# Kernel tuning notes

Hardware: AMD Instinct MI355X
Metric: run time of the kernel (lower is better)

Reference implementation:

```python
import jax, jax.numpy as jnp
import numpy as np

B, C, T, F = 2, 256, 1024, 64
N, HID = 4, 64


def setup_inputs() -> dict:
    key = jax.random.key(0)
    ks = jax.random.split(key, 9)
    s = 0.02
    return {
        "x": jax.random.normal(ks[0], (B, C, T, F), dtype=jnp.float32),
        "Wq": jax.random.normal(ks[1], (N, HID, C), dtype=jnp.float32) * s,
        "bq": jnp.zeros((N, HID), dtype=jnp.float32),
        "Wk": jax.random.normal(ks[2], (N, HID, C), dtype=jnp.float32) * s,
        "bk": jnp.zeros((N, HID), dtype=jnp.float32),
        "Wv": jax.random.normal(ks[3], (N, C // N, C), dtype=jnp.float32) * s,
        "bv": jnp.zeros((N, C // N), dtype=jnp.float32),
        "Wp": jax.random.normal(ks[4], (C, C), dtype=jnp.float32) * s,
        "bp": jnp.zeros((C,), dtype=jnp.float32),
    }


def reference(x, Wq, bq, Wk, bk, Wv, bv, Wp, bp):
    b, c, t, f = x.shape
    n = Wq.shape[0]
    # conv1x1 per head then torch: cat(dim=0) -> [N*b, h, t, f]; transpose(1,2); flatten -> [N*b, t, h*f]
    def proj(W, bias):
        h = W.shape[1]
        y = jnp.einsum('bctf,nhc->nbthf', x, W) + bias[:, None, None, :, None]
        return y.reshape(n * b, t, h * f)

    Q = proj(Wq, bq)                       # [N*b, t, hid*f]
    K = proj(Wk, bk)                       # [N*b, t, hid*f]
    V = proj(Wv, bv)                       # [N*b, t, (c/N)*f]

    scale = 1.0 / jnp.sqrt(jnp.asarray(Q.shape[-1], dtype=x.dtype))
    attn = jax.nn.softmax(jnp.einsum('mte,mse->mts', Q, K) * scale, axis=2)
    Vo = jnp.einsum('mts,msd->mtd', attn, V)             # [N*b, t, c*f/N]

    # torch: reshape(b*N, t, c*f//N).transpose(1,2).view(N,b,c//N,t,f).transpose(0,1).view(b,c,t,f)
    Vo = Vo.transpose(0, 2, 1)                            # [N*b, c*f/N, t]
    Vo = Vo.reshape(n, b, c // n, t, f)
    Vo = jnp.swapaxes(Vo, 0, 1).reshape(b, c, t, f)

    out = jnp.einsum('bctf,oc->botf', Vo, Wp) + bp[None, :, None, None]
    return out + x
```

## Files before the change

kernel.cpp:

```cpp
#include <hip/hip_runtime.h>

#define DI __device__ __forceinline__

static constexpr int B_ = 2;
static constexpr int C_ = 256;
static constexpr int T_ = 1024;
static constexpr int F_ = 64;
static constexpr int M_ = 8;
static constexpr int E_ = 4096;
static constexpr float SCALE_ = 1.0f / 64.0f;

typedef __attribute__((ext_vector_type(8))) short bf16x8;
typedef __attribute__((ext_vector_type(4))) float f32x4;

DI unsigned short bf16_rne(float f) {
    unsigned int u = __float_as_uint(f);
    return (unsigned short)((u + 0x7FFFu + ((u >> 16) & 1u)) >> 16);
}
DI float bf2f(unsigned short h) { return __uint_as_float(((unsigned int)h) << 16); }
DI ushort4 pack4(float a, float b, float c, float d) {
    return make_ushort4(bf16_rne(a), bf16_rne(b), bf16_rne(c), bf16_rne(d));
}
DI float4 up4(ushort4 u) {
    return make_float4(bf2f(u.x), bf2f(u.y), bf2f(u.z), bf2f(u.w));
}

DI void gload_lds16(const unsigned short* g, unsigned short* l) {
    __builtin_amdgcn_global_load_lds(
        (const __attribute__((address_space(1))) unsigned int*)g,
        (__attribute__((address_space(3))) unsigned int*)l, 16, 0, 0);
}

DI void mfma16(f32x4& acc, bf16x8 a, bf16x8 b) {
    asm("v_mfma_f32_16x16x32_bf16 %0, %1, %2, %0" : "+v"(acc) : "v"(a), "v"(b));
}

__global__ __launch_bounds__(256) void wconv_kernel(
    const float* __restrict__ Wq, const float* __restrict__ Wk,
    const float* __restrict__ Wv, const float* __restrict__ Wp,
    const float* __restrict__ bq, const float* __restrict__ bk,
    const float* __restrict__ bv,
    unsigned short* __restrict__ Wall, unsigned short* __restrict__ Wpb,
    float* __restrict__ bias_all)
{
    const int tid = (int)threadIdx.x;
    const int bid = (int)blockIdx.x;
    if (bid < 192) {
        const int idx = (bid * 256 + tid) * 4;
        const int proj = idx >> 16, rem = idx & 65535;
        const float* src = proj == 0 ? Wq : (proj == 1 ? Wk : Wv);
        float4 v = *(const float4*)(src + rem);
        *(ushort4*)(Wall + idx) = pack4(v.x, v.y, v.z, v.w);
        const int gid = bid * 256 + tid;
        if (gid < 768) {
            float bb = gid < 256 ? bq[gid] : (gid < 512 ? bk[gid - 256] : bv[gid - 512]);
            bias_all[gid] = bb;
        }
    } else {
        const int idx = ((bid - 192) * 256 + tid) * 4;
        float4 v = *(const float4*)(Wp + idx);
        *(ushort4*)(Wpb + idx) = pack4(v.x, v.y, v.z, v.w);
    }
}

__global__ __launch_bounds__(256) void qkv_two(
    const float* __restrict__ x, const unsigned short* __restrict__ Wall,
    const float* __restrict__ bias_all, unsigned short* __restrict__ outQ)
{
    const int wgid = (int)blockIdx.x;
    const int b = wgid >> 10, tft = wgid & 1023;
    const int tfbase = tft * 64;

    const int tid = (int)threadIdx.x;
    const int wid = tid >> 6, lane = tid & 63;
    const int wr = wid >> 1, wc = wid & 1;
    const int lo16 = lane & 15, hi4 = lane >> 4;

    __shared__ unsigned short As[4 * 64 * 64];
    __shared__ unsigned short Bs[128 * 64];

    {
        const int a = lane & 3, cg = lane >> 2;
        const int rowb = wid * 16 + a * 4;
        const float* xb = x + (size_t)b * (C_ * T_ * F_) + tfbase + rowb;
        const size_t cstep = 65536;

        float4 va[4], vb[4];
#pragma unroll
        for (int g = 0; g < 4; ++g)
            va[g] = *(const float4*)(xb + (size_t)(cg * 4 + g) * cstep);

#pragma unroll
        for (int cb = 0; cb < 4; ++cb) {
            if (cb < 3) {
                const int c0n = (cb + 1) * 64 + cg * 4;
#pragma unroll
                for (int g = 0; g < 4; ++g)
                    vb[g] = *(const float4*)(xb + (size_t)(c0n + g) * cstep);
            }
#pragma unroll
            for (int j = 0; j < 4; ++j) {
                const int row = rowb + j;
                const int phys = row * 64 + (((cg >> 1) ^ (row & 7)) << 3) + (cg & 1) * 4;
                float e0 = (&va[0].x)[j], e1 = (&va[1].x)[j];
                float e2 = (&va[2].x)[j], e3 = (&va[3].x)[j];
                *(ushort4*)&As[cb * 4096 + phys] = pack4(e0, e1, e2, e3);
            }
#pragma unroll
            for (int g = 0; g < 4; ++g) va[g] = vb[g];
        }
    }

    const int srow = lane >> 3;
    const int scol = ((lane & 7) ^ srow) * 8;
    const int tf0 = tfbase + wr * 32;

    __syncthreads();

    for (int ntl = 0; ntl < 6; ++ntl) {
        const int nbase = ntl * 128;
        const unsigned short* brow = Wall + (size_t)nbase * 256;
        f32x4 acc[2][4] = {};

        for (int kc = 0; kc < 4; ++kc) {
#pragma unroll
            for (int i = 0; i < 4; ++i) {
                const int rb = wid * 32 + i * 8;
                gload_lds16(brow + (size_t)(rb + srow) * 256 + kc * 64 + scol,
                            &Bs[rb * 64]);
            }
            __syncthreads();
#pragma unroll
            for (int kk = 0; kk < 2; ++kk) {
                const int hc = (kk * 32 + hi4 * 8) ^ ((lane & 7) << 3);
                bf16x8 a[2], bb[4];
#pragma unroll
                for (int mi = 0; mi < 2; ++mi)
                    a[mi] = *(const bf16x8*)&As[kc * 4096 + (wr * 32 + mi * 16 + lo16) * 64 + hc];
#pragma unroll
                for (int nj = 0; nj < 4; ++nj)
                    bb[nj] = *(const bf16x8*)&Bs[(wc * 64 + nj * 16 + lo16) * 64 + hc];
#pragma unroll
                for (int mi = 0; mi < 2; ++mi)
#pragma unroll
                    for (int nj = 0; nj < 4; ++nj)
                        mfma16(acc[mi][nj], a[mi], bb[nj]);
            }
            __syncthreads();
        }

        asm volatile("s_nop 7\n\ts_nop 7" ::: "memory");
#pragma unroll
        for (int nj = 0; nj < 4; ++nj) {
            const int r_col = nbase + wc * 64 + nj * 16 + lo16;
            const int projl = r_col >> 8;
            const int rr = r_col & 255;
            const int mrow = (rr >> 6) * 2 + b;
            const int h = rr & 63;
            const float bv = bias_all[r_col];
            unsigned short* dst0 = outQ + (size_t)projl * 33554432
                                 + (size_t)mrow * (T_ * E_) + h * 64;
#pragma unroll
            for (int mi = 0; mi < 2; ++mi) {
                const int tf = tf0 + mi * 16 + hi4 * 4;
                const int t = tf >> 6, f = tf & 63;
                *(ushort4*)(dst0 + (size_t)t * E_ + f) =
                    pack4(acc[mi][nj][0] + bv, acc[mi][nj][1] + bv,
                          acc[mi][nj][2] + bv, acc[mi][nj][3] + bv);
            }
        }
    }
}

__global__ __launch_bounds__(256) void scores_mfma(
    const unsigned short* __restrict__ Q, const unsigned short* __restrict__ K,
    unsigned short* __restrict__ S)
{
    const int orig = (int)blockIdx.x;
    const int wg = (orig & 7) * 64 + (orig >> 3);
    const int m = wg >> 6;
    const int rest = wg & 63;
    const int sbase = (rest & 7) * 128;
    const int tbase = (rest >> 3) * 128;
    const int tid = (int)threadIdx.x;
    const int wid = tid >> 6, lane = tid & 63;
    const int wr = wid >> 1, wc = wid & 1;
    const int lo16 = lane & 15, hi4 = lane >> 4;

    __shared__ unsigned short As[128 * 64];
    __shared__ unsigned short Bs[128 * 64];

    f32x4 acc[4][4] = {};

    const unsigned short* qrow = Q + ((size_t)m * T_ + tbase) * E_;
    const unsigned short* krow = K + ((size_t)m * T_ + sbase) * E_;

    const int srow = lane >> 3;
    const int scol = ((lane & 7) ^ srow) * 8;

    for (int eb = 0; eb < E_; eb += 64) {
#pragma unroll
        for (int i = 0; i < 4; ++i) {
            const int rb = wid * 32 + i * 8;
            gload_lds16(qrow + (size_t)(rb + srow) * E_ + eb + scol, &As[rb * 64]);
            gload_lds16(krow + (size_t)(rb + srow) * E_ + eb + scol, &Bs[rb * 64]);
        }
        __syncthreads();
#pragma unroll
        for (int kk = 0; kk < 2; ++kk) {
            const int hc = (kk * 32 + hi4 * 8) ^ ((lane & 7) << 3);
            bf16x8 a[4], bb[4];
#pragma unroll
            for (int mi = 0; mi < 4; ++mi)
                a[mi] = *(const bf16x8*)&As[(wr * 64 + mi * 16 + lo16) * 64 + hc];
#pragma unroll
            for (int nj = 0; nj < 4; ++nj)
                bb[nj] = *(const bf16x8*)&Bs[(wc * 64 + nj * 16 + lo16) * 64 + hc];
#pragma unroll
            for (int mi = 0; mi < 4; ++mi)
#pragma unroll
                for (int nj = 0; nj < 4; ++nj)
                    mfma16(acc[mi][nj], a[mi], bb[nj]);
        }
        __syncthreads();
    }

    asm volatile("s_nop 7\n\ts_nop 7" ::: "memory");
#pragma unroll
    for (int mi = 0; mi < 4; ++mi)
#pragma unroll
        for (int r = 0; r < 4; ++r) {
            int trow = tbase + wr * 64 + mi * 16 + hi4 * 4 + r;
            unsigned short* sp = S + ((size_t)m * T_ + trow) * T_ + sbase + wc * 64 + lo16;
#pragma unroll
            for (int nj = 0; nj < 4; ++nj)
                sp[nj * 16] = bf16_rne(acc[mi][nj][r] * SCALE_);
        }
}

__global__ __launch_bounds__(256) void softmax_kernel(
    const unsigned short* __restrict__ S, unsigned short* __restrict__ A)
{
    const size_t rowoff = ((size_t)blockIdx.y * T_ + blockIdx.x) * T_;
    const int tid = (int)threadIdx.x;
    const int wid = tid >> 6, lane = tid & 63;

    __shared__ float redmx[4];
    __shared__ float redsm[4];

    float4 v = up4(*(const ushort4*)(S + rowoff + tid * 4));
    float mx = fmaxf(fmaxf(v.x, v.y), fmaxf(v.z, v.w));
#pragma unroll
    for (int off = 32; off > 0; off >>= 1) mx = fmaxf(mx, __shfl_xor(mx, off));
    if (lane == 0) redmx[wid] = mx;
    __syncthreads();
    mx = fmaxf(fmaxf(redmx[0], redmx[1]), fmaxf(redmx[2], redmx[3]));

    float e0 = __expf(v.x - mx), e1 = __expf(v.y - mx);
    float e2 = __expf(v.z - mx), e3 = __expf(v.w - mx);
    float sm = (e0 + e1) + (e2 + e3);
#pragma unroll
    for (int off = 32; off > 0; off >>= 1) sm += __shfl_xor(sm, off);
    if (lane == 0) redsm[wid] = sm;
    __syncthreads();
    sm = (redsm[0] + redsm[1]) + (redsm[2] + redsm[3]);
    float inv = 1.0f / sm;
    *(ushort4*)(A + rowoff + tid * 4) = pack4(e0 * inv, e1 * inv, e2 * inv, e3 * inv);
}

__global__ __launch_bounds__(256) void vt_kernel(
    const unsigned short* __restrict__ V, unsigned short* __restrict__ Vt)
{
    const int m = blockIdx.z;
    const int d0 = blockIdx.x * 64;
    const int s0 = blockIdx.y * 64;
    const int tid = (int)threadIdx.x;
    __shared__ unsigned short ts[64][68];

    const unsigned short* vp = V + (size_t)m * T_ * E_;
#pragma unroll
    for (int it = 0; it < 4; ++it) {
        int idx = it * 256 + tid;
        int sl = idx >> 4, d4 = (idx & 15) * 4;
        *(ushort4*)&ts[sl][d4] = *(const ushort4*)&vp[(size_t)(s0 + sl) * E_ + d0 + d4];
    }
    __syncthreads();
    unsigned short* op = Vt + (size_t)m * E_ * T_;
    const int dl = tid >> 2, s16 = (tid & 3) * 16;
#pragma unroll
    for (int q = 0; q < 4; ++q) {
        int s4 = s16 + q * 4;
        ushort4 v = make_ushort4(ts[s4][dl], ts[s4+1][dl], ts[s4+2][dl], ts[s4+3][dl]);
        *(ushort4*)&op[(size_t)(d0 + dl) * T_ + s0 + s4] = v;
    }
}

__global__ __launch_bounds__(256) void pv_mfma(
    const unsigned short* __restrict__ A, const unsigned short* __restrict__ Vt,
    unsigned short* __restrict__ G)
{
    const int orig = (int)blockIdx.x;
    const int wg = (orig & 7) * 256 + (orig >> 3);
    const int m = wg >> 8;
    const int rest = wg & 255;
    const int dbase = (rest & 31) * 128;
    const int tbase = (rest >> 5) * 128;
    const int nh = m >> 1, b = m & 1;
    const int tid = (int)threadIdx.x;
    const int wid = tid >> 6, lane = tid & 63;
    const int wr = wid >> 1, wc = wid & 1;
    const int lo16 = lane & 15, hi4 = lane >> 4;

    __shared__ unsigned short As[128 * 64];
    __shared__ unsigned short Bs[128 * 64];

    f32x4 acc[4][4] = {};

    const unsigned short* arow = A  + ((size_t)m * T_ + tbase) * T_;
    const unsigned short* vrow = Vt + (size_t)m * E_ * T_ + (size_t)dbase * T_;

    const int srow = lane >> 3;
    const int scol = ((lane & 7) ^ srow) * 8;

    for (int sb = 0; sb < T_; sb += 64) {
#pragma unroll
        for (int i = 0; i < 4; ++i) {
            const int rb = wid * 32 + i * 8;
            gload_lds16(arow + (size_t)(rb + srow) * T_ + sb + scol, &As[rb * 64]);
            gload_lds16(vrow + (size_t)(rb + srow) * T_ + sb + scol, &Bs[rb * 64]);
        }
        __syncthreads();
#pragma unroll
        for (int kk = 0; kk < 2; ++kk) {
            const int hc = (kk * 32 + hi4 * 8) ^ ((lane & 7) << 3);
            bf16x8 a[4], bb[4];
#pragma unroll
            for (int mi = 0; mi < 4; ++mi)
                a[mi] = *(const bf16x8*)&As[(wr * 64 + mi * 16 + lo16) * 64 + hc];
#pragma unroll
            for (int nj = 0; nj < 4; ++nj)
                bb[nj] = *(const bf16x8*)&Bs[(wc * 64 + nj * 16 + lo16) * 64 + hc];
#pragma unroll
            for (int mi = 0; mi < 4; ++mi)
#pragma unroll
                for (int nj = 0; nj < 4; ++nj)
                    mfma16(acc[mi][nj], a[mi], bb[nj]);
        }
        __syncthreads();
    }

    asm volatile("s_nop 7\n\ts_nop 7" ::: "memory");
    const int cb   = nh * 64 + (dbase >> 6) + wc;
    const int t2lo = (tbase >> 6) + wr;
#pragma unroll
    for (int mi = 0; mi < 4; ++mi) {
        const int tl = mi * 16 + hi4 * 4;
#pragma unroll
        for (int nj = 0; nj < 4; ++nj) {
            const int d63 = nj * 16 + lo16;
            size_t addr = (((size_t)(b * 256 + cb)) * 1024 + d63 * 16 + t2lo) * 64 + tl;
            *(ushort4*)&G[addr] = pack4(acc[mi][nj][0], acc[mi][nj][1],
                                        acc[mi][nj][2], acc[mi][nj][3]);
        }
    }
}

__global__ __launch_bounds__(256) void gt_kernel(
    const unsigned short* __restrict__ G, unsigned short* __restrict__ GT)
{
    const int tf0 = blockIdx.x * 64;
    const int c0  = blockIdx.y * 64;
    const int b   = blockIdx.z;
    const int tid = (int)threadIdx.x;
    __shared__ unsigned short ts[64][68];

    const unsigned short* gb = G + (size_t)(b * 256 + c0) * 65536 + tf0;
#pragma unroll
    for (int it = 0; it < 4; ++it) {
        int idx = it * 256 + tid;
        int cl = idx >> 4, tf4 = (idx & 15) * 4;
        *(ushort4*)&ts[cl][tf4] = *(const ushort4*)(gb + (size_t)cl * 65536 + tf4);
    }
    __syncthreads();
    const int tfl = tid >> 2, c16 = (tid & 3) * 16;
    unsigned short* op = GT + ((size_t)b * 65536 + tf0 + tfl) * 256 + c0 + c16;
#pragma unroll
    for (int q = 0; q < 4; ++q) {
        int cl = c16 + q * 4;
        ushort4 v = make_ushort4(ts[cl][tfl], ts[cl+1][tfl], ts[cl+2][tfl], ts[cl+3][tfl]);
        *(ushort4*)(op + q * 4) = v;
    }
}

__global__ __launch_bounds__(256) void outproj_mfma(
    const unsigned short* __restrict__ GT, const unsigned short* __restrict__ Wpb,
    const float* __restrict__ bp, const float* __restrict__ x,
    float* __restrict__ out)
{
    const int tfbase = blockIdx.x * 128;
    const int obase  = blockIdx.y * 128;
    const int b      = blockIdx.z;
    const int tid = (int)threadIdx.x;
    const int wid = tid >> 6, lane = tid & 63;
    const int wr = wid >> 1, wc = wid & 1;
    const int lo16 = lane & 15, hi4 = lane >> 4;

    __shared__ unsigned short As[128 * 64];
    __shared__ unsigned short Bs[128 * 64];

    f32x4 acc[4][4] = {};

    const unsigned short* arow = GT + ((size_t)b * 65536 + tfbase) * 256;
    const unsigned short* brow = Wpb + (size_t)obase * 256;

    const int srow = lane >> 3;
    const int scol = ((lane & 7) ^ srow) * 8;

    for (int cb = 0; cb < 256; cb += 64) {
#pragma unroll
        for (int i = 0; i < 4; ++i) {
            const int rb = wid * 32 + i * 8;
            gload_lds16(arow + (size_t)(rb + srow) * 256 + cb + scol, &As[rb * 64]);
            gload_lds16(brow + (size_t)(rb + srow) * 256 + cb + scol, &Bs[rb * 64]);
        }
        __syncthreads();
#pragma unroll
        for (int kk = 0; kk < 2; ++kk) {
            const int hc = (kk * 32 + hi4 * 8) ^ ((lane & 7) << 3);
            bf16x8 a[4], bb[4];
#pragma unroll
            for (int mi = 0; mi < 4; ++mi)
                a[mi] = *(const bf16x8*)&As[(wr * 64 + mi * 16 + lo16) * 64 + hc];
#pragma unroll
            for (int nj = 0; nj < 4; ++nj)
                bb[nj] = *(const bf16x8*)&Bs[(wc * 64 + nj * 16 + lo16) * 64 + hc];
#pragma unroll
            for (int mi = 0; mi < 4; ++mi)
#pragma unroll
                for (int nj = 0; nj < 4; ++nj)
                    mfma16(acc[mi][nj], a[mi], bb[nj]);
        }
        __syncthreads();
    }

    asm volatile("s_nop 7\n\ts_nop 7" ::: "memory");
#pragma unroll
    for (int nj = 0; nj < 4; ++nj) {
        const int o = obase + wc * 64 + nj * 16 + lo16;
        const float bias = bp[o];
        const size_t rowb = ((size_t)(b * 256 + o)) * 65536;
#pragma unroll
        for (int mi = 0; mi < 4; ++mi) {
            const int tf = tfbase + wr * 64 + mi * 16 + hi4 * 4;
            float4 xv = *(const float4*)(x + rowb + tf);
            float4 r = make_float4(acc[mi][nj][0] + bias + xv.x,
                                   acc[mi][nj][1] + bias + xv.y,
                                   acc[mi][nj][2] + bias + xv.z,
                                   acc[mi][nj][3] + bias + xv.w);
            *(float4*)(out + rowb + tf) = r;
        }
    }
}

extern "C" void kernel_launch(void* const* d_in, const int* in_sizes, int n_in,
                              void* d_out, int out_size, void* d_ws, size_t ws_size,
                              hipStream_t stream) {
    const float* x  = (const float*)d_in[0];
    const float* Wq = (const float*)d_in[1];
    const float* bq = (const float*)d_in[2];
    const float* Wk = (const float*)d_in[3];
    const float* bk = (const float*)d_in[4];
    const float* Wv = (const float*)d_in[5];
    const float* bv = (const float*)d_in[6];
    const float* Wp = (const float*)d_in[7];
    const float* bp = (const float*)d_in[8];
    float* out = (float*)d_out;

    char* ws = (char*)d_ws;
    unsigned short* Q    = (unsigned short*)(ws);
    unsigned short* K    = (unsigned short*)(ws + 67108864);
    unsigned short* V    = (unsigned short*)(ws + 134217728);
    unsigned short* S    = (unsigned short*)(ws + 201326592);
    unsigned short* A    = (unsigned short*)(ws + 218103808);
    unsigned short* Wall = (unsigned short*)(ws + 234881024);
    float* bias_all      = (float*)(ws + 235274240);
    unsigned short* Wpb  = (unsigned short*)(ws + 235277312);
    unsigned short* Vt = K;
    unsigned short* G  = Q;
    unsigned short* GT = V;

    wconv_kernel<<<256, 256, 0, stream>>>(Wq, Wk, Wv, Wp, bq, bk, bv, Wall, Wpb, bias_all);
    qkv_two<<<2048, 256, 0, stream>>>(x, Wall, bias_all, Q);
    scores_mfma<<<512, 256, 0, stream>>>(Q, K, S);
    softmax_kernel<<<dim3(T_, M_), 256, 0, stream>>>(S, A);
    vt_kernel<<<dim3(64, 16, M_), 256, 0, stream>>>(V, Vt);
    pv_mfma<<<2048, 256, 0, stream>>>(A, Vt, G);
    gt_kernel<<<dim3(1024, 4, 2), 256, 0, stream>>>(G, GT);
    outproj_mfma<<<dim3(512, 2, 2), 256, 0, stream>>>(GT, Wpb, bp, x, out);
}
```

Baseline: 417.4 us.

## Load QKV weight fragments directly from global into registers, drop LDS B tile

The QKV projection kernel no longer stages weight tiles in shared memory. Each wave now owns 32 output columns across all 64 rows, reading its bf16 weight fragments straight from global/L2 into registers. This removes the LDS staging loads and both barriers per k-chunk. In exchange it loses cross-wave sharing of the B tile, relying on cache for the weight reads, and uses a different accumulator shape (4x2 instead of 2x4).

```diff
diff --git a/kernel.cpp b/kernel.cpp
--- a/kernel.cpp
+++ b/kernel.cpp
@@ -63,7 +63,7 @@
     }
 }
 
-__global__ __launch_bounds__(256) void qkv_two(
+__global__ __launch_bounds__(256) void qkv_three(
     const float* __restrict__ x, const unsigned short* __restrict__ Wall,
     const float* __restrict__ bias_all, unsigned short* __restrict__ outQ)
 {
@@ -73,11 +73,9 @@
 
     const int tid = (int)threadIdx.x;
     const int wid = tid >> 6, lane = tid & 63;
-    const int wr = wid >> 1, wc = wid & 1;
     const int lo16 = lane & 15, hi4 = lane >> 4;
 
     __shared__ unsigned short As[4 * 64 * 64];
-    __shared__ unsigned short Bs[128 * 64];
 
     {
         const int a = lane & 3, cg = lane >> 2;
@@ -111,48 +109,41 @@
         }
     }
 
-    const int srow = lane >> 3;
-    const int scol = ((lane & 7) ^ srow) * 8;
-    const int tf0 = tfbase + wr * 32;
-
     __syncthreads();
 
     for (int ntl = 0; ntl < 6; ++ntl) {
         const int nbase = ntl * 128;
-        const unsigned short* brow = Wall + (size_t)nbase * 256;
-        f32x4 acc[2][4] = {};
+        const unsigned short* wbase =
+            Wall + ((size_t)(nbase + wid * 32 + lo16)) * 256 + hi4 * 8;
+        f32x4 acc[4][2] = {};
 
         for (int kc = 0; kc < 4; ++kc) {
-#pragma unroll
-            for (int i = 0; i < 4; ++i) {
-                const int rb = wid * 32 + i * 8;
-                gload_lds16(brow + (size_t)(rb + srow) * 256 + kc * 64 + scol,
-                            &Bs[rb * 64]);
-            }
-            __syncthreads();
+            bf16x8 bfr[2][2];
+#pragma unroll
+            for (int kk = 0; kk < 2; ++kk)
+#pragma unroll
+                for (int nj = 0; nj < 2; ++nj)
+                    bfr[kk][nj] = *(const bf16x8*)(wbase + (size_t)nj * 16 * 256
+                                                   + kc * 64 + kk * 32);
 #pragma unroll
             for (int kk = 0; kk < 2; ++kk) {
                 const int hc = (kk * 32 + hi4 * 8) ^ ((lane & 7) << 3);
-                bf16x8 a[2], bb[4];
-#pragma unroll
-                for (int mi = 0; mi < 2; ++mi)
-                    a[mi] = *(const bf16x8*)&As[kc * 4096 + (wr * 32 + mi * 16 + lo16) * 64 + hc];
-#pragma unroll
-                for (int nj = 0; nj < 4; ++nj)
-                    bb[nj] = *(const bf16x8*)&Bs[(wc * 64 + nj * 16 + lo16) * 64 + hc];
-#pragma unroll
-                for (int mi = 0; mi < 2; ++mi)
-#pragma unroll
-                    for (int nj = 0; nj < 4; ++nj)
-                        mfma16(acc[mi][nj], a[mi], bb[nj]);
+                bf16x8 a[4];
+#pragma unroll
+                for (int mi = 0; mi < 4; ++mi)
+                    a[mi] = *(const bf16x8*)&As[kc * 4096 + (mi * 16 + lo16) * 64 + hc];
+#pragma unroll
+                for (int mi = 0; mi < 4; ++mi)
+#pragma unroll
+                    for (int nj = 0; nj < 2; ++nj)
+                        mfma16(acc[mi][nj], a[mi], bfr[kk][nj]);
             }
-            __syncthreads();
         }
 
         asm volatile("s_nop 7\n\ts_nop 7" ::: "memory");
 #pragma unroll
-        for (int nj = 0; nj < 4; ++nj) {
-            const int r_col = nbase + wc * 64 + nj * 16 + lo16;
+        for (int nj = 0; nj < 2; ++nj) {
+            const int r_col = nbase + wid * 32 + nj * 16 + lo16;
             const int projl = r_col >> 8;
             const int rr = r_col & 255;
             const int mrow = (rr >> 6) * 2 + b;
@@ -161,8 +152,8 @@
             unsigned short* dst0 = outQ + (size_t)projl * 33554432
                                  + (size_t)mrow * (T_ * E_) + h * 64;
 #pragma unroll
-            for (int mi = 0; mi < 2; ++mi) {
-                const int tf = tf0 + mi * 16 + hi4 * 4;
+            for (int mi = 0; mi < 4; ++mi) {
+                const int tf = tfbase + mi * 16 + hi4 * 4;
                 const int t = tf >> 6, f = tf & 63;
                 *(ushort4*)(dst0 + (size_t)t * E_ + f) =
                     pack4(acc[mi][nj][0] + bv, acc[mi][nj][1] + bv,
@@ -490,7 +481,7 @@
     unsigned short* GT = V;
 
     wconv_kernel<<<256, 256, 0, stream>>>(Wq, Wk, Wv, Wp, bq, bk, bv, Wall, Wpb, bias_all);
-    qkv_two<<<2048, 256, 0, stream>>>(x, Wall, bias_all, Q);
+    qkv_three<<<2048, 256, 0, stream>>>(x, Wall, bias_all, Q);
     scores_mfma<<<512, 256, 0, stream>>>(Q, K, S);
     softmax_kernel<<<dim3(T_, M_), 256, 0, stream>>>(S, A);
     vt_kernel<<<dim3(64, 16, M_), 256, 0, stream>>>(V, Vt);
```

After: 432.7 us. +3.7%, slower.
